# Optimization experiments

Hardware: AMD Instinct MI355X
Metric: run time of the kernel (lower is better)

Reference implementation:

```python
import jax, jax.numpy as jnp
import numpy as np

N_STATIONS = 276
CONTEXT_LEN = 384  # args.context_len * 2
TARGET_LEN = 96
BATCH = 4096


def setup_inputs() -> dict:
    key = jax.random.key(0)
    k1, k2, k3, k4, k5, k6 = jax.random.split(key, 6)
    z = jax.random.normal(k1, (BATCH, CONTEXT_LEN), dtype=jnp.float32)
    stations = jax.random.randint(k2, (BATCH,), 0, N_STATIONS, dtype=jnp.int64)
    # per-station Linear params (nn.Linear(context_len, target_len) x n_stations)
    lim = 1.0 / np.sqrt(CONTEXT_LEN)
    W = jax.random.uniform(k3, (N_STATIONS, TARGET_LEN, CONTEXT_LEN), jnp.float32, -lim, lim)
    b = jax.random.uniform(k4, (N_STATIONS, TARGET_LEN), jnp.float32, -lim, lim)
    loc = jax.random.normal(k5, (N_STATIONS,), dtype=jnp.float32)
    scale = jax.random.uniform(k6, (N_STATIONS,), jnp.float32, 0.5, 2.0)
    return {"z": z, "stations": stations, "W": W, "b": b, "loc": loc, "scale": scale}


def reference(z, stations, W, b, loc, scale):
    # norm: (z - loc[i]) / scale[i]
    loc_i = loc[stations][:, None]      # (bs, 1)
    scale_i = scale[stations][:, None]  # (bs, 1)
    zn = (z - loc_i) / scale_i          # (bs, context_len)
    # per-sample station-specific Linear: batched GEMV via gathered weights
    out = jnp.einsum("boi,bi->bo", W[stations], zn) + b[stations]  # (bs, target_len)
    # denorm then softplus
    out = out * scale_i + loc_i
    return jax.nn.softplus(out)
```

## Files before the change

### kernel.cpp

```cpp
#include <hip/hip_runtime.h>
#include <hip/hip_bf16.h>
#include <math.h>

#define N_STATIONS 276
#define CTX 384
#define TGT 96
#define BATCH 4096
#define NT_MAX 532
#define NTASK (NT_MAX * 6)
#define CPX (NTASK / 8)

#define META_OFF 8192
#define ZF_OFF   262144

typedef __attribute__((ext_vector_type(8))) short bf16x8;
typedef __attribute__((ext_vector_type(4))) float f32x4;

__device__ __forceinline__ short f2bf(float f) {
    return (short)__builtin_bit_cast(unsigned short, __float2bfloat16(f));
}

__global__ __launch_bounds__(1024) void build_lists(
    const int* __restrict__ stations, int* __restrict__ ws)
{
    __shared__ int cnt[N_STATIONS], cnt2[N_STATIONS];
    __shared__ int poff[N_STATIONS + 1], tpoff[N_STATIONS + 1];
    const int tid = threadIdx.x;
    for (int i = tid; i < N_STATIONS; i += 1024) { cnt[i] = 0; cnt2[i] = 0; }
    __syncthreads();
    for (int b = tid; b < BATCH; b += 1024) atomicAdd(&cnt[stations[b]], 1);
    __syncthreads();
    if (tid < 64) {
        int run = 0, trun = 0;
        for (int base = 0; base < N_STATIONS; base += 64) {
            const int i = base + tid;
            int c  = (i < N_STATIONS) ? cnt[i] : 0;
            int v  = c, tv = (c + 15) >> 4;
#pragma unroll
            for (int off = 1; off < 64; off <<= 1) {
                int u  = __shfl_up(v, off, 64);
                int tu = __shfl_up(tv, off, 64);
                if (tid >= off) { v += u; tv += tu; }
            }
            if (i < N_STATIONS) { poff[i + 1] = run + v; tpoff[i + 1] = trun + tv; }
            run  += __shfl(v, 63, 64);
            trun += __shfl(tv, 63, 64);
        }
        if (tid == 0) { poff[0] = 0; tpoff[0] = 0; }
    }
    __syncthreads();
    int* order = ws + 1024;
    for (int b = tid; b < BATCH; b += 1024) {
        int s = stations[b];
        int p = atomicAdd(&cnt2[s], 1);
        order[poff[s] + p] = b;
    }
    for (int i = tid; i < N_STATIONS; i += 1024) {
        int n = (cnt[i] + 15) >> 4, base = tpoff[i];
        for (int t = 0; t < n; ++t) ws[1 + base + t] = (i << 16) | t;
    }
    if (tid <= N_STATIONS) ws[5120 + tid] = poff[tid];
    if (tid == 0) ws[0] = tpoff[N_STATIONS];
}

__global__ __launch_bounds__(256) void zstage(
    const float* __restrict__ z,
    const float* __restrict__ loc,
    const float* __restrict__ scale,
    int* __restrict__ ws)
{
    const int ntiles = ws[0];
    const int tb = blockIdx.x;
    if (tb >= ntiles) return;

    const int pk = ws[1 + tb];
    const int s  = pk >> 16;
    const int tt = pk & 0xFFFF;
    const int* order   = ws + 1024;
    const int* offsets = ws + 5120;
    const int start = offsets[s];
    const int m     = offsets[s + 1] - start;

    const float lc = loc[s], inv = 1.0f / scale[s], nb = -lc * inv;

    int* rec = ws + META_OFF + tb * 32;
    const int t = threadIdx.x;
    if (t < 16) {
        int j = tt * 16 + t; if (j > m - 1) j = m - 1;
        rec[2 + t] = order[start + j];
    }
    if (t == 0) { rec[0] = s; int mr = m - tt * 16; rec[1] = mr > 16 ? 16 : mr; }

    unsigned short* zt = (unsigned short*)(ws + ZF_OFF) + (size_t)tb * 6144;
    for (int q = t; q < 768; q += 256) {
        const int kstep = q >> 6, lane = q & 63;
        const int sample = lane & 15;
        const int kb = kstep * 32 + (lane >> 4) * 8;
        int j = tt * 16 + sample; if (j > m - 1) j = m - 1;
        const float* zr = z + (size_t)order[start + j] * CTX + kb;
        float4 a0 = *(const float4*)zr;
        float4 a1 = *(const float4*)(zr + 4);
        float f[8] = {a0.x, a0.y, a0.z, a0.w, a1.x, a1.y, a1.z, a1.w};
        union { unsigned short u[8]; uint4 v; } o;
#pragma unroll
        for (int i = 0; i < 8; ++i)
            o.u[i] = (unsigned short)f2bf(fmaf(f[i], inv, nb));
        *(uint4*)(zt + (size_t)q * 8) = o.v;
    }
}

__global__ __launch_bounds__(64, 4) void nlinear_hot(
    const float* __restrict__ W,
    const float* __restrict__ bias,
    const float* __restrict__ loc,
    const float* __restrict__ scale,
    const int*   __restrict__ ws,
    float*       __restrict__ out)
{
    const int ntasks = ws[0] * 6;
    const int b0 = blockIdx.x;
    const int b  = (b0 & 7) * CPX + (b0 >> 3);
    if (b >= ntasks) return;

    const int tile = b / 6;
    const int nt   = b - tile * 6;

    const int* rec = ws + META_OFF + tile * 32;
    const int s    = rec[0];
    const int mrem = rec[1];

    const int l  = threadIdx.x;
    const int lr = l & 15;
    const int kh = (l >> 4) * 8;

    const float* wr = W + ((size_t)s * TGT + nt * 16 + lr) * CTX + kh;
    const unsigned short* zt = (const unsigned short*)(ws + ZF_OFF) + (size_t)tile * 6144;

    f32x4 acc = {0.f, 0.f, 0.f, 0.f};
    float4 wc0 = *(const float4*)(wr);
    float4 wc1 = *(const float4*)(wr + 4);
    bf16x8 za  = *(const bf16x8*)(zt + (size_t)l * 8);

#pragma unroll
    for (int kk = 0; kk < 12; ++kk) {
        float4 wn0, wn1; bf16x8 zn_;
        if (kk < 11) {
            wn0 = *(const float4*)(wr + (kk + 1) * 32);
            wn1 = *(const float4*)(wr + (kk + 1) * 32 + 4);
            zn_ = *(const bf16x8*)(zt + ((size_t)(kk + 1) * 64 + l) * 8);
        }
        bf16x8 bh;
        bh[0] = f2bf(wc0.x); bh[1] = f2bf(wc0.y);
        bh[2] = f2bf(wc0.z); bh[3] = f2bf(wc0.w);
        bh[4] = f2bf(wc1.x); bh[5] = f2bf(wc1.y);
        bh[6] = f2bf(wc1.z); bh[7] = f2bf(wc1.w);
        acc = __builtin_amdgcn_mfma_f32_16x16x32_bf16(za, bh, acc, 0, 0, 0);
        if (kk < 11) { wc0 = wn0; wc1 = wn1; za = zn_; }
    }

    const float sc = scale[s], lc = loc[s];
    const float bv = bias[(size_t)s * TGT + nt * 16 + lr];
    const int rbase = (l >> 4) * 4;
#pragma unroll
    for (int r = 0; r < 4; ++r) {
        const int jj = rbase + r;
        if (jj < mrem) {
            const int oid = rec[2 + jj];
            float v = (acc[r] + bv) * sc + lc;
            out[(size_t)oid * TGT + nt * 16 + lr] =
                fmaxf(v, 0.f) + log1pf(expf(-fabsf(v)));
        }
    }
}

extern "C" void kernel_launch(void* const* d_in, const int* in_sizes, int n_in,
                              void* d_out, int out_size, void* d_ws, size_t ws_size,
                              hipStream_t stream) {
    const float* z        = (const float*)d_in[0];
    const int*   stations = (const int*)  d_in[1];
    const float* W        = (const float*)d_in[2];
    const float* bias     = (const float*)d_in[3];
    const float* loc      = (const float*)d_in[4];
    const float* scale    = (const float*)d_in[5];
    float* out = (float*)d_out;
    int* ws = (int*)d_ws;

    build_lists<<<1, 1024, 0, stream>>>(stations, ws);
    zstage<<<NT_MAX, 256, 0, stream>>>(z, loc, scale, ws);
    nlinear_hot<<<NTASK, 64, 0, stream>>>(W, bias, loc, scale, ws, out);
}
```

Measured before the change: 30.88 us.

## Split K across two wavefronts per block and reduce partial sums in LDS

The GEMV kernel now uses 128 threads per block. Each wavefront handles half of the 384-long context dimension, and the partial MFMA accumulators are combined through shared memory before the epilogue. All W and z loads for each half are issued up front into registers instead of a one-step software prefetch. This shortens the serial MFMA chain per wave and exposes more memory-level parallelism. In exchange it adds a block barrier, LDS traffic and more registers per thread.

```diff
diff --git a/kernel.cpp b/kernel.cpp
--- a/kernel.cpp
+++ b/kernel.cpp
@@ -109,7 +109,7 @@
     }
 }
 
-__global__ __launch_bounds__(64, 4) void nlinear_hot(
+__global__ __launch_bounds__(128, 4) void nlinear_hot2(
     const float* __restrict__ W,
     const float* __restrict__ bias,
     const float* __restrict__ loc,
@@ -117,6 +117,8 @@
     const int*   __restrict__ ws,
     float*       __restrict__ out)
 {
+    __shared__ float part[16][17];
+
     const int ntasks = ws[0] * 6;
     const int b0 = blockIdx.x;
     const int b  = (b0 & 7) * CPX + (b0 >> 3);
@@ -129,46 +131,54 @@
     const int s    = rec[0];
     const int mrem = rec[1];
 
-    const int l  = threadIdx.x;
-    const int lr = l & 15;
-    const int kh = (l >> 4) * 8;
-
-    const float* wr = W + ((size_t)s * TGT + nt * 16 + lr) * CTX + kh;
-    const unsigned short* zt = (const unsigned short*)(ws + ZF_OFF) + (size_t)tile * 6144;
+    const int tid = threadIdx.x;
+    const int l   = tid & 63;
+    const int h   = tid >> 6;
+    const int lr  = l & 15;
+    const int kh  = (l >> 4) * 8;
+
+    const float* wr = W + ((size_t)s * TGT + nt * 16 + lr) * CTX + h * 192 + kh;
+    const unsigned short* zt = (const unsigned short*)(ws + ZF_OFF)
+                             + (size_t)tile * 6144 + (size_t)h * 6 * 64 * 8;
+
+    float4 wv[12];
+    bf16x8 za[6];
+#pragma unroll
+    for (int kk = 0; kk < 6; ++kk) {
+        wv[2 * kk]     = *(const float4*)(wr + kk * 32);
+        wv[2 * kk + 1] = *(const float4*)(wr + kk * 32 + 4);
+        za[kk]         = *(const bf16x8*)(zt + (size_t)kk * 64 * 8 + (size_t)l * 8);
+    }
 
     f32x4 acc = {0.f, 0.f, 0.f, 0.f};
-    float4 wc0 = *(const float4*)(wr);
-    float4 wc1 = *(const float4*)(wr + 4);
-    bf16x8 za  = *(const bf16x8*)(zt + (size_t)l * 8);
-
-#pragma unroll
-    for (int kk = 0; kk < 12; ++kk) {
-        float4 wn0, wn1; bf16x8 zn_;
-        if (kk < 11) {
-            wn0 = *(const float4*)(wr + (kk + 1) * 32);
-            wn1 = *(const float4*)(wr + (kk + 1) * 32 + 4);
-            zn_ = *(const bf16x8*)(zt + ((size_t)(kk + 1) * 64 + l) * 8);
-        }
+#pragma unroll
+    for (int kk = 0; kk < 6; ++kk) {
         bf16x8 bh;
-        bh[0] = f2bf(wc0.x); bh[1] = f2bf(wc0.y);
-        bh[2] = f2bf(wc0.z); bh[3] = f2bf(wc0.w);
-        bh[4] = f2bf(wc1.x); bh[5] = f2bf(wc1.y);
-        bh[6] = f2bf(wc1.z); bh[7] = f2bf(wc1.w);
-        acc = __builtin_amdgcn_mfma_f32_16x16x32_bf16(za, bh, acc, 0, 0, 0);
-        if (kk < 11) { wc0 = wn0; wc1 = wn1; za = zn_; }
-    }
-
-    const float sc = scale[s], lc = loc[s];
-    const float bv = bias[(size_t)s * TGT + nt * 16 + lr];
+        bh[0] = f2bf(wv[2 * kk].x);     bh[1] = f2bf(wv[2 * kk].y);
+        bh[2] = f2bf(wv[2 * kk].z);     bh[3] = f2bf(wv[2 * kk].w);
+        bh[4] = f2bf(wv[2 * kk + 1].x); bh[5] = f2bf(wv[2 * kk + 1].y);
+        bh[6] = f2bf(wv[2 * kk + 1].z); bh[7] = f2bf(wv[2 * kk + 1].w);
+        acc = __builtin_amdgcn_mfma_f32_16x16x32_bf16(za[kk], bh, acc, 0, 0, 0);
+    }
+
     const int rbase = (l >> 4) * 4;
-#pragma unroll
-    for (int r = 0; r < 4; ++r) {
-        const int jj = rbase + r;
-        if (jj < mrem) {
-            const int oid = rec[2 + jj];
-            float v = (acc[r] + bv) * sc + lc;
-            out[(size_t)oid * TGT + nt * 16 + lr] =
-                fmaxf(v, 0.f) + log1pf(expf(-fabsf(v)));
+    if (h == 1) {
+#pragma unroll
+        for (int r = 0; r < 4; ++r) part[rbase + r][lr] = acc[r];
+    }
+    __syncthreads();
+    if (h == 0) {
+        const float sc = scale[s], lc = loc[s];
+        const float bv = bias[(size_t)s * TGT + nt * 16 + lr];
+#pragma unroll
+        for (int r = 0; r < 4; ++r) {
+            const int jj = rbase + r;
+            if (jj < mrem) {
+                const int oid = rec[2 + jj];
+                float v = (acc[r] + part[rbase + r][lr] + bv) * sc + lc;
+                out[(size_t)oid * TGT + nt * 16 + lr] =
+                    fmaxf(v, 0.f) + log1pf(expf(-fabsf(v)));
+            }
         }
     }
 }
@@ -187,5 +197,5 @@
 
     build_lists<<<1, 1024, 0, stream>>>(stations, ws);
     zstage<<<NT_MAX, 256, 0, stream>>>(z, loc, scale, ws);
-    nlinear_hot<<<NTASK, 64, 0, stream>>>(W, bias, loc, scale, ws, out);
-}
+    nlinear_hot2<<<NTASK, 128, 0, stream>>>(W, bias, loc, scale, ws, out);
+}
```

Result: slower. 31.50 us (+2.0%).
